# Performance work log

Hardware: AMD Instinct MI355X
Metric: run time of the kernel (lower is better)

The kernel has to match this reference:

```python
import jax, jax.numpy as jnp
import numpy as np

EMBED_DIM = 1024
NUM_HEADS = 16
HEAD_DIM = EMBED_DIM // NUM_HEADS


def setup_inputs() -> dict:
    key = jax.random.key(0)
    k_x, k_qw, k_qb, k_ow, k_ob = jax.random.split(key, 5)
    B, T, C = 4, 2048, EMBED_DIM
    s = 1.0 / np.sqrt(C)
    return {
        "x": jax.random.normal(k_x, (B, T, C), dtype=jnp.float32),
        # torch nn.Linear weights: [out_features, in_features]
        "qkv_w": jax.random.uniform(k_qw, (3 * C, C), jnp.float32, -s, s),
        "qkv_b": jax.random.uniform(k_qb, (3 * C,), jnp.float32, -s, s),
        "out_w": jax.random.uniform(k_ow, (C, C), jnp.float32, -s, s),
        "out_b": jax.random.uniform(k_ob, (C,), jnp.float32, -s, s),
    }


def reference(x, qkv_w, qkv_b, out_w, out_b):
    B, T, C = x.shape
    H, D = NUM_HEADS, HEAD_DIM
    qkv = x @ qkv_w.T + qkv_b                      # [B,T,3C]
    qkv = qkv.reshape(B, T, 3, H, D).transpose(2, 0, 3, 1, 4)  # [3,B,H,T,D]
    Q, K, V = qkv[0], qkv[1], qkv[2]
    scores = jnp.einsum("bhtd,bhsd->bhts", Q, K) / np.sqrt(D).astype(np.float32)
    causal = jnp.triu(jnp.ones((T, T), dtype=bool), k=1)        # mask future
    scores = jnp.where(causal, -jnp.inf, scores)
    attn_weights = jax.nn.softmax(scores, axis=-1)              # [B,H,T,T]
    out = jnp.einsum("bhts,bhsd->bhtd", attn_weights, V)
    out = out.transpose(0, 2, 1, 3).reshape(B, T, C)
    return out @ out_w.T + out_b, attn_weights
```

## Files before the change

kernel.cpp:

```cpp
#include <hip/hip_runtime.h>
#include <cstdint>
#include <cstddef>

#define Bq  4
#define Tq  2048
#define Cq  1024
#define Hq  16
#define Dq  64
#define BTq 8192
#define C3q 3072

using bf16x8 = __attribute__((ext_vector_type(8))) short;
using f32x4  = __attribute__((ext_vector_type(4))) float;
using us4    = __attribute__((ext_vector_type(4))) unsigned short;

__device__ __forceinline__ unsigned short f2bf(float f) {
  unsigned u = __builtin_bit_cast(unsigned, f);
  return (unsigned short)((u + 0x7fffu + ((u >> 16) & 1u)) >> 16);
}
__device__ __forceinline__ float bf2f(unsigned short h) {
  return __builtin_bit_cast(float, (unsigned)h << 16);
}

__device__ __forceinline__ void gload_lds16(const void* g, void* l) {
  __builtin_amdgcn_global_load_lds(
      (const __attribute__((address_space(1))) void*)g,
      (__attribute__((address_space(3))) void*)l, 16, 0, 0);
}

__global__ __launch_bounds__(256) void cvt_kernel(const float* __restrict__ src,
                                                  unsigned short* __restrict__ dst, int n4) {
  int i = blockIdx.x * 256 + threadIdx.x;
  int stride = gridDim.x * 256;
  for (; i < n4; i += stride) {
    float4 v = reinterpret_cast<const float4*>(src)[i];
    us4 o = { f2bf(v.x), f2bf(v.y), f2bf(v.z), f2bf(v.w) };
    reinterpret_cast<us4*>(dst)[i] = o;
  }
}

template<int EPI>
__global__ __launch_bounds__(256) void gemm128(
    const unsigned short* __restrict__ A, const unsigned short* __restrict__ Bw,
    const float* __restrict__ bias,
    unsigned short* __restrict__ Qb, unsigned short* __restrict__ Kb,
    unsigned short* __restrict__ Vtb, float* __restrict__ Cout,
    int M, int N, int K)
{
  __shared__ unsigned short As[128][32];
  __shared__ unsigned short Bs[128][32];
  const int n0 = blockIdx.x * 128, m0 = blockIdx.y * 128;
  const int tid = threadIdx.x;
  const int w = tid >> 6, l = tid & 63, r = l & 15, g = l >> 4;
  const int wm = w >> 1, wn = w & 1;
  const int ldRow = tid >> 2, ldCol = (tid & 3) * 8;
  f32x4 acc[4][4] = {};

  const unsigned short* Ar0 = A  + (size_t)(m0 +      ldRow) * K + ldCol;
  const unsigned short* Ar1 = A  + (size_t)(m0 + 64 + ldRow) * K + ldCol;
  const unsigned short* Br0 = Bw + (size_t)(n0 +      ldRow) * K + ldCol;
  const unsigned short* Br1 = Bw + (size_t)(n0 + 64 + ldRow) * K + ldCol;
  char* Ab0 = (char*)&As[0][0]        + w * 1024;
  char* Ab1 = (char*)&As[0][0] + 4096 + w * 1024;
  char* Bb0 = (char*)&Bs[0][0]        + w * 1024;
  char* Bb1 = (char*)&Bs[0][0] + 4096 + w * 1024;

  for (int k0 = 0; k0 < K; k0 += 32) {
    __syncthreads();
    gload_lds16(Ar0 + k0, Ab0);
    gload_lds16(Ar1 + k0, Ab1);
    gload_lds16(Br0 + k0, Bb0);
    gload_lds16(Br1 + k0, Bb1);
    __syncthreads();
    bf16x8 a[4], b[4];
    #pragma unroll
    for (int i = 0; i < 4; ++i) a[i] = *(const bf16x8*)&As[wm*64 + i*16 + r][g*8];
    #pragma unroll
    for (int j = 0; j < 4; ++j) b[j] = *(const bf16x8*)&Bs[wn*64 + j*16 + r][g*8];
    #pragma unroll
    for (int i = 0; i < 4; ++i)
      #pragma unroll
      for (int j = 0; j < 4; ++j)
        acc[i][j] = __builtin_amdgcn_mfma_f32_16x16x32_bf16(a[i], b[j], acc[i][j], 0, 0, 0);
  }

  if (EPI == 0) {
    const int which = n0 >> 10;
    #pragma unroll
    for (int i = 0; i < 4; ++i)
      #pragma unroll
      for (int j = 0; j < 4; ++j) {
        int gc  = n0 + wn*64 + j*16 + r;
        int gr0 = m0 + wm*64 + i*16 + 4*g;
        float bv = bias[gc];
        int hd = gc & 1023;
        int h = hd >> 6, d = hd & 63;
        if (which == 2) {
          int b = gr0 >> 11, t0 = gr0 & 2047;
          int bh = b*Hq + h;
          us4 pk = { f2bf(acc[i][j][0] + bv), f2bf(acc[i][j][1] + bv),
                     f2bf(acc[i][j][2] + bv), f2bf(acc[i][j][3] + bv) };
          *(us4*)&Vtb[(size_t)(bh*Dq + d)*Tq + t0] = pk;
        } else {
          unsigned short* dst = which ? Kb : Qb;
          #pragma unroll
          for (int jj = 0; jj < 4; ++jj) {
            int gr = gr0 + jj;
            int b = gr >> 11, t = gr & 2047;
            int bh = b*Hq + h;
            dst[(size_t)(bh*Tq + t)*Dq + d] = f2bf(acc[i][j][jj] + bv);
          }
        }
      }
  } else {
    #pragma unroll
    for (int i = 0; i < 4; ++i)
      #pragma unroll
      for (int j = 0; j < 4; ++j) {
        int gc = n0 + wn*64 + j*16 + r;
        float bv = bias[gc];
        #pragma unroll
        for (int jj = 0; jj < 4; ++jj) {
          int gr = m0 + wm*64 + i*16 + 4*g + jj;
          Cout[(size_t)gr * N + gc] = acc[i][j][jj] + bv;
        }
      }
  }
}

#define PROWB 4224
#define XMASK(row_) ((((row_) & 7) << 4) ^ ((((row_) >> 2) & 3) << 5))

__global__ __launch_bounds__(512, 4) void attn_kernel(
    const unsigned short* __restrict__ Qb, const unsigned short* __restrict__ Kb,
    const unsigned short* __restrict__ Vtb,
    float* __restrict__ attn, unsigned short* __restrict__ ctxb)
{
  __shared__ __align__(16) unsigned short P[16][2112];
  __shared__ float red[8][32];
  __shared__ float invl_s[32];
  __shared__ f32x4 Cred[4][2][64];

  const int p  = blockIdx.x;
  const int bh = blockIdx.y;
  const int tid = threadIdx.x, w = tid >> 6, l = tid & 63, r = l & 15, g = l >> 4;
  const int qbA = p * 16, qbB = (127 - p) * 16;
  const int NA = (qbA + 16 + 31) >> 5;
  const int NB = (qbB + 16 + 31) >> 5;
  const int LAc = NA * 32, LBc = NB * 32;

  const unsigned short* Qp = Qb  + (size_t)bh * Tq * Dq;
  const unsigned short* Kp = Kb  + (size_t)bh * Tq * Dq;
  const unsigned short* Vp = Vtb + (size_t)bh * Dq * Tq;
  char* Pmut = (char*)&P[0][0];

  bf16x8 aqA0 = *(const bf16x8*)&Qp[(size_t)(qbA + r)*Dq      + g*8];
  bf16x8 aqA1 = *(const bf16x8*)&Qp[(size_t)(qbA + r)*Dq + 32 + g*8];
  bf16x8 aqB0 = *(const bf16x8*)&Qp[(size_t)(qbB + r)*Dq      + g*8];
  bf16x8 aqB1 = *(const bf16x8*)&Qp[(size_t)(qbB + r)*Dq + 32 + g*8];

  float lsumA[4] = {0.f,0.f,0.f,0.f}, lsumB[4] = {0.f,0.f,0.f,0.f};

#define LOADK(ci_, D00, D01, D10, D11)                                              \
  {                                                                                 \
    int cj_ = ((ci_) < NA) ? (ci_) : (ci_) - NA;                                    \
    int k0c_ = cj_ * 32;                                                            \
    D00 = *(const bf16x8*)&Kp[(size_t)(k0c_ + r)*Dq      + g*8];                    \
    D01 = *(const bf16x8*)&Kp[(size_t)(k0c_ + r)*Dq + 32 + g*8];                    \
    D10 = *(const bf16x8*)&Kp[(size_t)(k0c_ + 16 + r)*Dq      + g*8];               \
    D11 = *(const bf16x8*)&Kp[(size_t)(k0c_ + 16 + r)*Dq + 32 + g*8];               \
  }

  {
    bf16x8 k00, k01, k10, k11, n00, n01, n10, n11;
    int ci = w;
    if (ci < 65) LOADK(ci, k00, k01, k10, k11);
    for (; ci < 65; ci += 8) {
      if (ci + 8 < 65) LOADK(ci + 8, n00, n01, n10, n11);
      const bool isA = ci < NA;
      const int cj  = isA ? ci : ci - NA;
      const int k0c = cj * 32;
      const int qb_ = isA ? qbA : qbB;
      const int cb_ = isA ? k0c : LAc + k0c;
      bf16x8 q0_ = isA ? aqA0 : aqB0;
      bf16x8 q1_ = isA ? aqA1 : aqB1;
      f32x4 z = {0.f,0.f,0.f,0.f};
      __builtin_amdgcn_s_setprio(1);
      f32x4 s0 = __builtin_amdgcn_mfma_f32_16x16x32_bf16(q0_, k00, z, 0, 0, 0);
      s0 = __builtin_amdgcn_mfma_f32_16x16x32_bf16(q1_, k01, s0, 0, 0, 0);
      f32x4 s1 = __builtin_amdgcn_mfma_f32_16x16x32_bf16(q0_, k10, z, 0, 0, 0);
      s1 = __builtin_amdgcn_mfma_f32_16x16x32_bf16(q1_, k11, s1, 0, 0, 0);
      __builtin_amdgcn_s_setprio(0);
      float tch[4];
      #pragma unroll
      for (int jj = 0; jj < 4; ++jj) {
        int q = qb_ + 4*g + jj;
        float p0 = (k0c + r      <= q) ? __expf(s0[jj]*0.125f) : 0.f;
        float p1 = (k0c + 16 + r <= q) ? __expf(s1[jj]*0.125f) : 0.f;
        tch[jj] = p0 + p1;
        int row = 4*g + jj, xm = XMASK(row);
        *(unsigned short*)(Pmut + row*PROWB + (((cb_ + r)*2)      ^ xm)) = f2bf(p0);
        *(unsigned short*)(Pmut + row*PROWB + (((cb_ + 16 + r)*2) ^ xm)) = f2bf(p1);
      }
      if (isA) { lsumA[0]+=tch[0]; lsumA[1]+=tch[1]; lsumA[2]+=tch[2]; lsumA[3]+=tch[3]; }
      else     { lsumB[0]+=tch[0]; lsumB[1]+=tch[1]; lsumB[2]+=tch[2]; lsumB[3]+=tch[3]; }
      k00 = n00; k01 = n01; k10 = n10; k11 = n11;
    }
  }

  #pragma unroll
  for (int jj = 0; jj < 4; ++jj) {
    float sa = lsumA[jj], sb = lsumB[jj];
    #pragma unroll
    for (int off = 1; off < 16; off <<= 1) {
      sa += __shfl_xor(sa, off, 64);
      sb += __shfl_xor(sb, off, 64);
    }
    if (r == 0) { red[w][4*g + jj] = sa; red[w][16 + 4*g + jj] = sb; }
  }
  __syncthreads();
  if (tid < 32) {
    float s = 0.f;
    #pragma unroll
    for (int ww = 0; ww < 8; ++ww) s += red[ww][tid];
    invl_s[tid] = 1.f / s;
  }
  __syncthreads();

  {
    const int s16   = tid >> 8;
    const int row16 = (tid >> 4) & 15;
    const int seg   = (tid & 15) * 8;
    const int xm16  = XMASK(row16);
    const char* Prow = Pmut + row16 * PROWB;
    const int Lc    = s16 ? LBc : LAc;
    const int cbase = s16 ? LAc : 0;
    float inv = invl_s[s16*16 + row16];
    size_t ob = ((size_t)bh*Tq + (s16 ? qbB : qbA) + row16) * Tq;
    for (int cb = seg; cb < Tq; cb += 128) {
      f32x4 v0 = {0.f,0.f,0.f,0.f}, v1 = {0.f,0.f,0.f,0.f};
      if (cb < Lc) {
        bf16x8 pv = *(const bf16x8*)(Prow + (((cbase + cb)*2) ^ xm16));
        v0[0]=bf2f((unsigned short)pv[0])*inv; v0[1]=bf2f((unsigned short)pv[1])*inv;
        v0[2]=bf2f((unsigned short)pv[2])*inv; v0[3]=bf2f((unsigned short)pv[3])*inv;
        v1[0]=bf2f((unsigned short)pv[4])*inv; v1[1]=bf2f((unsigned short)pv[5])*inv;
        v1[2]=bf2f((unsigned short)pv[6])*inv; v1[3]=bf2f((unsigned short)pv[7])*inv;
      }
      __builtin_nontemporal_store(v0, (f32x4*)&attn[ob + cb]);
      __builtin_nontemporal_store(v1, (f32x4*)&attn[ob + cb + 4]);
    }
  }

  f32x4 coA = {0.f,0.f,0.f,0.f}, coB = {0.f,0.f,0.f,0.f};
  {
    const int dblk = w & 3, par = w >> 2;
    const char* Pr = Pmut + r * PROWB;
    const int xr = XMASK(r);
    const unsigned short* Vrow = &Vp[(size_t)(dblk*16 + r) * Tq];
    bf16x8 pa, bv, pan, bvn;
    int ci = par;
    {
      int cj = (ci < NA) ? ci : ci - NA;
      int cb = (ci < NA) ? ci*32 : LAc + cj*32;
      pa = *(const bf16x8*)(Pr + (((cb + g*8)*2) ^ xr));
      bv = *(const bf16x8*)&Vrow[cj*32 + g*8];
    }
    for (; ci < 65; ci += 2) {
      if (ci + 2 < 65) {
        int cn = ci + 2;
        int cj = (cn < NA) ? cn : cn - NA;
        int cb = (cn < NA) ? cn*32 : LAc + cj*32;
        pan = *(const bf16x8*)(Pr + (((cb + g*8)*2) ^ xr));
        bvn = *(const bf16x8*)&Vrow[cj*32 + g*8];
      }
      if (ci < NA) coA = __builtin_amdgcn_mfma_f32_16x16x32_bf16(pa, bv, coA, 0, 0, 0);
      else         coB = __builtin_amdgcn_mfma_f32_16x16x32_bf16(pa, bv, coB, 0, 0, 0);
      pa = pan; bv = bvn;
    }
    if (par == 1) { Cred[dblk][0][l] = coA; Cred[dblk][1][l] = coB; }
  }
  __syncthreads();
  if ((w >> 2) == 0) {
    const int dblk = w & 3;
    f32x4 cA = Cred[dblk][0][l], cB = Cred[dblk][1][l];
    coA[0]+=cA[0]; coA[1]+=cA[1]; coA[2]+=cA[2]; coA[3]+=cA[3];
    coB[0]+=cB[0]; coB[1]+=cB[1]; coB[2]+=cB[2]; coB[3]+=cB[3];
    const int b = bh >> 4, h = bh & 15;
    #pragma unroll
    for (int jj = 0; jj < 4; ++jj) {
      int tA = qbA + 4*g + jj;
      ctxb[(size_t)(b*Tq + tA)*Cq + h*Dq + dblk*16 + r] = f2bf(coA[jj] * invl_s[4*g + jj]);
      int tB = qbB + 4*g + jj;
      ctxb[(size_t)(b*Tq + tB)*Cq + h*Dq + dblk*16 + r] = f2bf(coB[jj] * invl_s[16 + 4*g + jj]);
    }
  }
#undef LOADK
}

extern "C" void kernel_launch(void* const* d_in, const int* in_sizes, int n_in,
                              void* d_out, int out_size, void* d_ws, size_t ws_size,
                              hipStream_t stream) {
  const float* x     = (const float*)d_in[0];
  const float* qkv_w = (const float*)d_in[1];
  const float* qkv_b = (const float*)d_in[2];
  const float* out_w = (const float*)d_in[3];
  const float* out_b = (const float*)d_in[4];
  float* out  = (float*)d_out;
  float* attn = out + (size_t)BTq * Cq;

  char* ws = (char*)d_ws;
  unsigned short* xb    = (unsigned short*)(ws);
  unsigned short* wqkvb = (unsigned short*)(ws + (16u << 20));
  unsigned short* woutb = (unsigned short*)(ws + (22u << 20));
  unsigned short* Qb    = (unsigned short*)(ws + (24u << 20));
  unsigned short* Kb    = (unsigned short*)(ws + (40u << 20));
  unsigned short* Vtb   = (unsigned short*)(ws + (56u << 20));
  unsigned short* ctxb  = (unsigned short*)(ws + (72u << 20));

  cvt_kernel<<<2048, 256, 0, stream>>>(x,     xb,    (BTq * Cq) / 4);
  cvt_kernel<<<1024, 256, 0, stream>>>(qkv_w, wqkvb, (C3q * Cq) / 4);
  cvt_kernel<<<512,  256, 0, stream>>>(out_w, woutb, (Cq * Cq) / 4);

  dim3 g1(C3q / 128, BTq / 128);
  gemm128<0><<<g1, 256, 0, stream>>>(xb, wqkvb, qkv_b, Qb, Kb, Vtb, nullptr, BTq, C3q, Cq);

  dim3 g2(64, Bq * Hq);
  attn_kernel<<<g2, 512, 0, stream>>>(Qb, Kb, Vtb, attn, ctxb);

  dim3 g3(Cq / 128, BTq / 128);
  gemm128<1><<<g3, 256, 0, stream>>>(ctxb, woutb, out_b, nullptr, nullptr, nullptr, out, BTq, Cq, Cq);
}
```

Before: 511.3 us.

## Specialize warps: half write attention probs, half compute P@V concurrently

Splits the eight wavefronts into two roles after the softmax normalization: waves 0-3 stream the normalized attention probabilities to global memory, while waves 4-7 each compute one 16-column D block of P@V over all chunks using two interleaved accumulators. This removes the LDS cross-wave reduction buffer and its extra barrier, and lets the store-bound attn write overlap with the MFMA work. The trade-off is that each role now runs on half as many waves, so the store phase issues twice as much per wave and the MFMA chain per wave is twice as long.

Result: no change. 504.7 us (-1.3%).

```diff
diff --git a/kernel.cpp b/kernel.cpp
--- a/kernel.cpp
+++ b/kernel.cpp
@@ -139,7 +139,6 @@
   __shared__ __align__(16) unsigned short P[16][2112];
   __shared__ float red[8][32];
   __shared__ float invl_s[32];
-  __shared__ f32x4 Cred[4][2][64];
 
   const int p  = blockIdx.x;
   const int bh = blockIdx.y;
@@ -227,71 +226,70 @@
   }
   __syncthreads();
 
-  {
-    const int s16   = tid >> 8;
-    const int row16 = (tid >> 4) & 15;
-    const int seg   = (tid & 15) * 8;
-    const int xm16  = XMASK(row16);
-    const char* Prow = Pmut + row16 * PROWB;
-    const int Lc    = s16 ? LBc : LAc;
-    const int cbase = s16 ? LAc : 0;
-    float inv = invl_s[s16*16 + row16];
-    size_t ob = ((size_t)bh*Tq + (s16 ? qbB : qbA) + row16) * Tq;
-    for (int cb = seg; cb < Tq; cb += 128) {
-      f32x4 v0 = {0.f,0.f,0.f,0.f}, v1 = {0.f,0.f,0.f,0.f};
-      if (cb < Lc) {
-        bf16x8 pv = *(const bf16x8*)(Prow + (((cbase + cb)*2) ^ xm16));
-        v0[0]=bf2f((unsigned short)pv[0])*inv; v0[1]=bf2f((unsigned short)pv[1])*inv;
-        v0[2]=bf2f((unsigned short)pv[2])*inv; v0[3]=bf2f((unsigned short)pv[3])*inv;
-        v1[0]=bf2f((unsigned short)pv[4])*inv; v1[1]=bf2f((unsigned short)pv[5])*inv;
-        v1[2]=bf2f((unsigned short)pv[6])*inv; v1[3]=bf2f((unsigned short)pv[7])*inv;
-      }
-      __builtin_nontemporal_store(v0, (f32x4*)&attn[ob + cb]);
-      __builtin_nontemporal_store(v1, (f32x4*)&attn[ob + cb + 4]);
-    }
-  }
-
-  f32x4 coA = {0.f,0.f,0.f,0.f}, coB = {0.f,0.f,0.f,0.f};
-  {
-    const int dblk = w & 3, par = w >> 2;
+  if (w < 4) {
+    #pragma unroll
+    for (int s = 0; s < 2; ++s) {
+      const int idx   = s * 256 + tid;
+      const int s16   = idx >> 8;
+      const int row16 = (idx >> 4) & 15;
+      const int seg   = (idx & 15) * 8;
+      const int xm16  = XMASK(row16);
+      const char* Prow = Pmut + row16 * PROWB;
+      const int Lc    = s16 ? LBc : LAc;
+      const int cbase = s16 ? LAc : 0;
+      float inv = invl_s[s16*16 + row16];
+      size_t ob = ((size_t)bh*Tq + (s16 ? qbB : qbA) + row16) * Tq;
+      for (int cb = seg; cb < Tq; cb += 128) {
+        f32x4 v0 = {0.f,0.f,0.f,0.f}, v1 = {0.f,0.f,0.f,0.f};
+        if (cb < Lc) {
+          bf16x8 pv = *(const bf16x8*)(Prow + (((cbase + cb)*2) ^ xm16));
+          v0[0]=bf2f((unsigned short)pv[0])*inv; v0[1]=bf2f((unsigned short)pv[1])*inv;
+          v0[2]=bf2f((unsigned short)pv[2])*inv; v0[3]=bf2f((unsigned short)pv[3])*inv;
+          v1[0]=bf2f((unsigned short)pv[4])*inv; v1[1]=bf2f((unsigned short)pv[5])*inv;
+          v1[2]=bf2f((unsigned short)pv[6])*inv; v1[3]=bf2f((unsigned short)pv[7])*inv;
+        }
+        __builtin_nontemporal_store(v0, (f32x4*)&attn[ob + cb]);
+        __builtin_nontemporal_store(v1, (f32x4*)&attn[ob + cb + 4]);
+      }
+    }
+  } else {
+    const int dblk = w - 4;
     const char* Pr = Pmut + r * PROWB;
     const int xr = XMASK(r);
     const unsigned short* Vrow = &Vp[(size_t)(dblk*16 + r) * Tq];
+    f32x4 coA0 = {0.f,0.f,0.f,0.f}, coA1 = {0.f,0.f,0.f,0.f};
+    f32x4 coB0 = {0.f,0.f,0.f,0.f}, coB1 = {0.f,0.f,0.f,0.f};
     bf16x8 pa, bv, pan, bvn;
-    int ci = par;
     {
-      int cj = (ci < NA) ? ci : ci - NA;
-      int cb = (ci < NA) ? ci*32 : LAc + cj*32;
-      pa = *(const bf16x8*)(Pr + (((cb + g*8)*2) ^ xr));
-      bv = *(const bf16x8*)&Vrow[cj*32 + g*8];
-    }
-    for (; ci < 65; ci += 2) {
-      if (ci + 2 < 65) {
-        int cn = ci + 2;
+      pa = *(const bf16x8*)(Pr + (((0 + g*8)*2) ^ xr));
+      bv = *(const bf16x8*)&Vrow[g*8];
+    }
+    for (int ci = 0; ci < 65; ++ci) {
+      if (ci + 1 < 65) {
+        int cn = ci + 1;
         int cj = (cn < NA) ? cn : cn - NA;
         int cb = (cn < NA) ? cn*32 : LAc + cj*32;
         pan = *(const bf16x8*)(Pr + (((cb + g*8)*2) ^ xr));
         bvn = *(const bf16x8*)&Vrow[cj*32 + g*8];
       }
-      if (ci < NA) coA = __builtin_amdgcn_mfma_f32_16x16x32_bf16(pa, bv, coA, 0, 0, 0);
-      else         coB = __builtin_amdgcn_mfma_f32_16x16x32_bf16(pa, bv, coB, 0, 0, 0);
+      if (ci < NA) {
+        if (ci & 1) coA1 = __builtin_amdgcn_mfma_f32_16x16x32_bf16(pa, bv, coA1, 0, 0, 0);
+        else        coA0 = __builtin_amdgcn_mfma_f32_16x16x32_bf16(pa, bv, coA0, 0, 0, 0);
+      } else {
+        if (ci & 1) coB1 = __builtin_amdgcn_mfma_f32_16x16x32_bf16(pa, bv, coB1, 0, 0, 0);
+        else        coB0 = __builtin_amdgcn_mfma_f32_16x16x32_bf16(pa, bv, coB0, 0, 0, 0);
+      }
       pa = pan; bv = bvn;
     }
-    if (par == 1) { Cred[dblk][0][l] = coA; Cred[dblk][1][l] = coB; }
-  }
-  __syncthreads();
-  if ((w >> 2) == 0) {
-    const int dblk = w & 3;
-    f32x4 cA = Cred[dblk][0][l], cB = Cred[dblk][1][l];
-    coA[0]+=cA[0]; coA[1]+=cA[1]; coA[2]+=cA[2]; coA[3]+=cA[3];
-    coB[0]+=cB[0]; coB[1]+=cB[1]; coB[2]+=cB[2]; coB[3]+=cB[3];
     const int b = bh >> 4, h = bh & 15;
     #pragma unroll
     for (int jj = 0; jj < 4; ++jj) {
       int tA = qbA + 4*g + jj;
-      ctxb[(size_t)(b*Tq + tA)*Cq + h*Dq + dblk*16 + r] = f2bf(coA[jj] * invl_s[4*g + jj]);
+      ctxb[(size_t)(b*Tq + tA)*Cq + h*Dq + dblk*16 + r] =
+          f2bf((coA0[jj] + coA1[jj]) * invl_s[4*g + jj]);
       int tB = qbB + 4*g + jj;
-      ctxb[(size_t)(b*Tq + tB)*Cq + h*Dq + dblk*16 + r] = f2bf(coB[jj] * invl_s[16 + 4*g + jj]);
+      ctxb[(size_t)(b*Tq + tB)*Cq + h*Dq + dblk*16 + r] =
+          f2bf((coB0[jj] + coB1[jj]) * invl_s[16 + 4*g + jj]);
     }
   }
 #undef LOADK
```
